# Kernel optimization log

Hardware: AMD Instinct MI355X
Metric: run time of the kernel (lower is better)

Reference implementation:

```python
import jax, jax.numpy as jnp
import numpy as np

DIM = 1024
CTX_DIM = 1024
HEADS = 16
HEAD_DIM = DIM // HEADS


def setup_inputs() -> dict:
    key = jax.random.key(0)
    ks = jax.random.split(key, 6)
    B, N, M = 2, 2048, 2048
    s = 0.02
    return {
        "x": jax.random.normal(ks[0], (B, N, DIM), dtype=jnp.float32),
        "context": jax.random.normal(ks[1], (B, M, CTX_DIM), dtype=jnp.float32),
        "W_q": jax.random.normal(ks[2], (DIM, DIM), dtype=jnp.float32) * s,
        "W_kv": jax.random.normal(ks[3], (CTX_DIM * 2, CTX_DIM), dtype=jnp.float32) * s,
        "W_proj": jax.random.normal(ks[4], (DIM, DIM), dtype=jnp.float32) * s,
        "b_proj": jax.random.normal(ks[5], (DIM,), dtype=jnp.float32) * s,
    }


def reference(x, context, W_q, W_kv, W_proj, b_proj):
    B, N, C = x.shape
    M = context.shape[1]
    scale = HEAD_DIM ** (-0.5)
    # q projection: [B,N,H,D]
    q = (x @ W_q.T).reshape(B, N, HEADS, HEAD_DIM) * scale
    # context kv projection: [B,M,2,H,D]
    kv = (context @ W_kv.T).reshape(B, M, 2, HEADS, HEAD_DIM)
    k = kv[:, :, 0]  # [B,M,H,D]
    v = kv[:, :, 0]  # NOTE: source uses qkv_context[0] for BOTH k and v (faithful)
    attn = jnp.einsum("bnhd,bmhd->bhnm", q, k)
    attn = jax.nn.softmax(attn, axis=-1)
    out = jnp.einsum("bhnm,bmhd->bnhd", attn, v).reshape(B, N, C)
    return out @ W_proj.T + b_proj
```

## Files before the change

### kernel.cpp

```cpp
#include <hip/hip_runtime.h>
#include <hip/hip_bf16.h>


typedef __bf16 bf16x8 __attribute__((ext_vector_type(8)));
typedef float f32x4 __attribute__((ext_vector_type(4)));
typedef float f32x16 __attribute__((ext_vector_type(16)));

static constexpr int kDIM = 1024;
static constexpr float kLog2e = 1.4426950408889634f;

__device__ inline unsigned short f2bf(float f) {
    union { float f; unsigned int u; } v; v.f = f;
    return (unsigned short)((v.u + 0x7FFFu + ((v.u >> 16) & 1u)) >> 16);
}

__device__ inline unsigned int pack2bf(float a, float b) {
    union { float f; unsigned int u; } ua, ub;
    ua.f = a; ub.f = b;
    return __builtin_amdgcn_perm(ub.u + 0x8000u, ua.u + 0x8000u, 0x07060302u);
}

__device__ inline void gload_lds16(const unsigned short* g, unsigned short* l) {
    __builtin_amdgcn_global_load_lds(
        (const __attribute__((address_space(1))) unsigned int*)g,
        (__attribute__((address_space(3))) unsigned int*)l, 16, 0, 0);
}

__global__ __launch_bounds__(256) void cast_all(
    const float* __restrict__ x, const float* __restrict__ ctx,
    const float* __restrict__ wq, const float* __restrict__ wkv,
    const float* __restrict__ wp,
    unsigned short* __restrict__ xb, unsigned short* __restrict__ cb,
    unsigned short* __restrict__ wqb, unsigned short* __restrict__ wkb,
    unsigned short* __restrict__ wpb)
{
    int j = blockIdx.x * 256 + threadIdx.x;
    const float* s; unsigned short* d;
    if (j < 1048576)                      { s = x;   d = xb;  }
    else if ((j -= 1048576) < 1048576)    { s = ctx; d = cb;  }
    else if ((j -= 1048576) < 262144)     { s = wq;  d = wqb; }
    else if ((j -= 262144) < 262144)      { s = wkv; d = wkb; }
    else if ((j -= 262144) < 262144)      { s = wp;  d = wpb; }
    else return;
    float4 f = ((const float4*)s)[j];
    ushort4 o;
    o.x = f2bf(f.x); o.y = f2bf(f.y); o.z = f2bf(f.z); o.w = f2bf(f.w);
    ((ushort4*)d)[j] = o;
}

__global__ __launch_bounds__(256, 4) void gemm_qk(
    const unsigned short* __restrict__ xb, const unsigned short* __restrict__ cb,
    const unsigned short* __restrict__ Wq, const unsigned short* __restrict__ Wkv,
    unsigned short* __restrict__ Qb, unsigned short* __restrict__ Kb,
    unsigned short* __restrict__ Ktb, float qscale, int Mctx)
{
    __shared__ unsigned short As[128 * 64];
    __shared__ unsigned short Bs[64 * 64];
    const int z = blockIdx.z;
    const unsigned short* A  = z ? cb : xb;
    const unsigned short* Bw = z ? Wkv : Wq;
    unsigned short* Cb = z ? Kb : Qb;
    const float scale = z ? 1.0f : qscale;

    const int tid = threadIdx.x;
    const int wave = tid >> 6, lane = tid & 63;
    const int g = lane >> 4, c = lane & 15;
    const int wm = (wave & 1) * 64, wn = (wave >> 1) * 32;
    const int bm = blockIdx.y * 128, bn = blockIdx.x * 64;

    const int srow = lane >> 3;
    const int scolsw = ((lane & 7) ^ (srow & 7)) * 8;
    const int x7 = c & 7;

    f32x4 acc[4][2];
    #pragma unroll
    for (int i = 0; i < 4; ++i)
        #pragma unroll
        for (int j = 0; j < 2; ++j)
            acc[i][j] = (f32x4){0.f, 0.f, 0.f, 0.f};

    for (int k0 = 0; k0 < kDIM; k0 += 64) {
        __syncthreads();
        #pragma unroll
        for (int t = 0; t < 4; ++t) {
            const int chunk = wave * 4 + t;
            gload_lds16(A + (size_t)(bm + chunk * 8 + srow) * kDIM + k0 + scolsw,
                        &As[chunk * 512]);
        }
        #pragma unroll
        for (int t = 0; t < 2; ++t) {
            const int chunk = wave * 2 + t;
            gload_lds16(Bw + (size_t)(bn + chunk * 8 + srow) * kDIM + k0 + scolsw,
                        &Bs[chunk * 512]);
        }
        __syncthreads();
        #pragma unroll
        for (int kc = 0; kc < 2; ++kc) {
            bf16x8 af[4], bfr[2];
            #pragma unroll
            for (int i = 0; i < 4; ++i)
                af[i] = *(const bf16x8*)&As[(wm + i * 16 + c) * 64 +
                                            ((kc * 4 + g) ^ x7) * 8];
            #pragma unroll
            for (int j = 0; j < 2; ++j)
                bfr[j] = *(const bf16x8*)&Bs[(wn + j * 16 + c) * 64 +
                                             ((kc * 4 + g) ^ x7) * 8];
            #pragma unroll
            for (int i = 0; i < 4; ++i)
                #pragma unroll
                for (int j = 0; j < 2; ++j)
                    acc[i][j] = __builtin_amdgcn_mfma_f32_16x16x32_bf16(
                        af[i], bfr[j], acc[i][j], 0, 0, 0);
        }
    }

    #pragma unroll
    for (int i = 0; i < 4; ++i) {
        #pragma unroll
        for (int j = 0; j < 2; ++j) {
            const int r0 = bm + wm + i * 16 + 4 * g;
            const int cc = bn + wn + j * 16 + c;
            float v0 = acc[i][j][0] * scale;
            float v1 = acc[i][j][1] * scale;
            float v2 = acc[i][j][2] * scale;
            float v3 = acc[i][j][3] * scale;
            Cb[(size_t)(r0 + 0) * kDIM + cc] = f2bf(v0);
            Cb[(size_t)(r0 + 1) * kDIM + cc] = f2bf(v1);
            Cb[(size_t)(r0 + 2) * kDIM + cc] = f2bf(v2);
            Cb[(size_t)(r0 + 3) * kDIM + cc] = f2bf(v3);
            if (z) {
                const int bb = r0 / Mctx, n0 = r0 % Mctx;
                const int hh = cc >> 6, d = cc & 63;
                ushort4 pk;
                pk.x = f2bf(v0); pk.y = f2bf(v1); pk.z = f2bf(v2); pk.w = f2bf(v3);
                *(ushort4*)&Ktb[((size_t)((bb * 16 + hh) * 64 + d)) * Mctx + n0] = pk;
            }
        }
    }
}

__global__ __launch_bounds__(256, 4) void gemm_proj(
    const unsigned short* __restrict__ Ab, const unsigned short* __restrict__ Wp,
    const float* __restrict__ bias, float* __restrict__ out)
{
    __shared__ unsigned short As[64 * 64];
    __shared__ unsigned short Bs[64 * 64];
    const int tid = threadIdx.x;
    const int wave = tid >> 6, lane = tid & 63;
    const int g = lane >> 4, c = lane & 15;
    const int wm = (wave & 1) * 32, wn = (wave >> 1) * 32;
    const int bm = blockIdx.y * 64, bn = blockIdx.x * 64;

    const int srow = lane >> 3;
    const int scolsw = ((lane & 7) ^ (srow & 7)) * 8;
    const int x7 = c & 7;

    f32x4 acc[2][2];
    #pragma unroll
    for (int i = 0; i < 2; ++i)
        #pragma unroll
        for (int j = 0; j < 2; ++j)
            acc[i][j] = (f32x4){0.f, 0.f, 0.f, 0.f};

    for (int k0 = 0; k0 < kDIM; k0 += 64) {
        __syncthreads();
        #pragma unroll
        for (int t = 0; t < 2; ++t) {
            const int chunk = wave * 2 + t;
            const int row = chunk * 8 + srow;
            gload_lds16(Ab + (size_t)(bm + row) * kDIM + k0 + scolsw, &As[chunk * 512]);
            gload_lds16(Wp + (size_t)(bn + row) * kDIM + k0 + scolsw, &Bs[chunk * 512]);
        }
        __syncthreads();
        #pragma unroll
        for (int kc = 0; kc < 2; ++kc) {
            bf16x8 af[2], bfr[2];
            #pragma unroll
            for (int i = 0; i < 2; ++i)
                af[i] = *(const bf16x8*)&As[(wm + i * 16 + c) * 64 +
                                            ((kc * 4 + g) ^ x7) * 8];
            #pragma unroll
            for (int j = 0; j < 2; ++j)
                bfr[j] = *(const bf16x8*)&Bs[(wn + j * 16 + c) * 64 +
                                             ((kc * 4 + g) ^ x7) * 8];
            #pragma unroll
            for (int i = 0; i < 2; ++i)
                #pragma unroll
                for (int j = 0; j < 2; ++j)
                    acc[i][j] = __builtin_amdgcn_mfma_f32_16x16x32_bf16(
                        af[i], bfr[j], acc[i][j], 0, 0, 0);
        }
    }

    #pragma unroll
    for (int i = 0; i < 2; ++i) {
        #pragma unroll
        for (int j = 0; j < 2; ++j) {
            const int r0 = bm + wm + i * 16 + 4 * g;
            const int cc = bn + wn + j * 16 + c;
            const float bv = bias[cc];
            #pragma unroll
            for (int ii = 0; ii < 4; ++ii)
                out[(size_t)(r0 + ii) * kDIM + cc] = acc[i][j][ii] + bv;
        }
    }
}

__global__ __launch_bounds__(512, 4) void attn_mfma_v5(
    const unsigned short* __restrict__ Q,
    const unsigned short* __restrict__ K,
    const unsigned short* __restrict__ Kt,
    unsigned short* __restrict__ O, int N, int M)
{
    __shared__ unsigned short smem[18432];
    unsigned short* Ks  = smem;
    unsigned short* Kts = smem + 64 * 72;
    unsigned short* Ps  = smem + 2 * 64 * 72;

    const int b = blockIdx.z, h = blockIdx.y, q0 = blockIdx.x * 128;
    const int tid = threadIdx.x;
    const int w = tid >> 6, lane = tid & 63;
    const int strip = w >> 1, kh = w & 1;
    const int ql = lane & 31, l5 = lane >> 5;

    const unsigned short* Qrow = Q + (size_t)(b * N + q0 + strip * 32 + ql) * kDIM + h * 64;
    const unsigned short* Kb = K + (size_t)b * M * kDIM + h * 64;
    const unsigned short* Ktb = Kt + (size_t)((b * 16 + h) * 64) * M;

    bf16x8 bq[4];
    #pragma unroll
    for (int kc = 0; kc < 4; ++kc)
        bq[kc] = *(const bf16x8*)(Qrow + kc * 16 + l5 * 8);

    f32x16 ot[2];
    #pragma unroll
    for (int dt = 0; dt < 2; ++dt)
        #pragma unroll
        for (int r = 0; r < 16; ++r) ot[dt][r] = 0.f;
    float lac = 0.f;

    const int srow = tid >> 3, scol = (tid & 7) * 8;
    unsigned short* prow = &Ps[(strip * 32 + ql) * 72 + kh * 32];

    for (int k0 = 0; k0 < M; k0 += 64) {
        __syncthreads();
        *(uint4*)&Ks[srow * 72 + scol] =
            *(const uint4*)(Kb + (size_t)(k0 + srow) * kDIM + scol);
        *(uint4*)&Kts[srow * 72 + scol] =
            *(const uint4*)(Ktb + (size_t)srow * M + k0 + scol);
        __syncthreads();

        f32x16 st;
        #pragma unroll
        for (int r = 0; r < 16; ++r) st[r] = 0.f;
        #pragma unroll
        for (int kc = 0; kc < 4; ++kc) {
            bf16x8 ak = *(const bf16x8*)&Ks[(kh * 32 + ql) * 72 + kc * 16 + l5 * 8];
            st = __builtin_amdgcn_mfma_f32_32x32x16_bf16(ak, bq[kc], st, 0, 0, 0);
        }

        float pr[16];
        #pragma unroll
        for (int r = 0; r < 16; ++r) {
            pr[r] = __builtin_amdgcn_exp2f(st[r]);
            lac += pr[r];
        }
        unsigned int dw[8];
        #pragma unroll
        for (int p = 0; p < 8; ++p) dw[p] = pack2bf(pr[2 * p], pr[2 * p + 1]);
        #pragma unroll
        for (int pp = 0; pp < 4; ++pp)
            *(uint2*)&prow[8 * pp + 4 * l5] = make_uint2(dw[2 * pp], dw[2 * pp + 1]);

        #pragma unroll
        for (int kc2 = 0; kc2 < 2; ++kc2) {
            bf16x8 bp = *(const bf16x8*)&prow[kc2 * 16 + l5 * 8];
            #pragma unroll
            for (int dt = 0; dt < 2; ++dt) {
                bf16x8 av = *(const bf16x8*)&Kts[(dt * 32 + ql) * 72 + kh * 32 + kc2 * 16 + l5 * 8];
                ot[dt] = __builtin_amdgcn_mfma_f32_32x32x16_bf16(av, bp, ot[dt], 0, 0, 0);
            }
        }
    }

    float lw = lac + __shfl_xor(lac, 32);
    float* Om = (float*)smem;
    float* Lm = Om + 128 * 68;
    const int qi = strip * 32 + ql;

    __syncthreads();
    if (kh == 1) {
        #pragma unroll
        for (int dt = 0; dt < 2; ++dt)
            #pragma unroll
            for (int rr = 0; rr < 4; ++rr)
                *(f32x4*)&Om[qi * 68 + dt * 32 + 8 * rr + 4 * l5] =
                    (f32x4){ot[dt][4 * rr], ot[dt][4 * rr + 1],
                            ot[dt][4 * rr + 2], ot[dt][4 * rr + 3]};
        if (l5 == 0) Lm[qi] = lw;
    }
    __syncthreads();
    if (kh == 0) {
        const float inv = 1.0f / (lw + Lm[qi]);
        unsigned short* Ob = O + (size_t)(b * N + q0 + qi) * kDIM + h * 64;
        #pragma unroll
        for (int dt = 0; dt < 2; ++dt)
            #pragma unroll
            for (int rr = 0; rr < 4; ++rr) {
                f32x4 pv = *(const f32x4*)&Om[qi * 68 + dt * 32 + 8 * rr + 4 * l5];
                ushort4 u;
                u.x = f2bf((ot[dt][4 * rr]     + pv[0]) * inv);
                u.y = f2bf((ot[dt][4 * rr + 1] + pv[1]) * inv);
                u.z = f2bf((ot[dt][4 * rr + 2] + pv[2]) * inv);
                u.w = f2bf((ot[dt][4 * rr + 3] + pv[3]) * inv);
                *(ushort4*)(Ob + dt * 32 + 8 * rr + 4 * l5) = u;
            }
    }
}

extern "C" void kernel_launch(void* const* d_in, const int* in_sizes, int n_in,
                              void* d_out, int out_size, void* d_ws, size_t ws_size,
                              hipStream_t stream)
{
    const float* x      = (const float*)d_in[0];
    const float* ctxp   = (const float*)d_in[1];
    const float* W_q    = (const float*)d_in[2];
    const float* W_kv   = (const float*)d_in[3];
    const float* W_proj = (const float*)d_in[4];
    const float* b_proj = (const float*)d_in[5];
    float* out = (float*)d_out;

    const int B = 2, N = 2048, M = 2048;
    const int BN = B * N;
    const int SQ = kDIM * kDIM;

    unsigned short* p = (unsigned short*)d_ws;
    unsigned short* xb  = p; p += (size_t)BN * kDIM;
    unsigned short* cb  = p; p += (size_t)BN * kDIM;
    unsigned short* wqb = p; p += SQ;
    unsigned short* wkb = p; p += SQ;
    unsigned short* wpb = p; p += SQ;
    unsigned short* Qb  = p; p += (size_t)BN * kDIM;
    unsigned short* Kb  = p; p += (size_t)BN * kDIM;
    unsigned short* Ktb = p; p += (size_t)BN * kDIM;
    unsigned short* Ab  = xb;

    hipLaunchKernelGGL(cast_all, dim3(11264), dim3(256), 0, stream,
                       x, ctxp, W_q, W_kv, W_proj, xb, cb, wqb, wkb, wpb);
    hipLaunchKernelGGL(gemm_qk, dim3(kDIM / 64, BN / 128, 2), dim3(256), 0, stream,
                       xb, cb, wqb, wkb, Qb, Kb, Ktb, 0.125f * kLog2e, M);
    hipLaunchKernelGGL(attn_mfma_v5, dim3(N / 128, 16, B), dim3(512), 0, stream,
                       Qb, Kb, Ktb, Ab, N, M);
    hipLaunchKernelGGL(gemm_proj, dim3(kDIM / 64, BN / 64), dim3(256), 0, stream,
                       Ab, wpb, b_proj, out);
}
```

Measured before the change: 187.1 us.

## Prefetch attention K tiles into registers, enlarge proj GEMM tile, use hardware bf16 pack

The attention kernel now loads the next K and K-transposed tiles into registers while the current tile is being computed, so global load latency can overlap the MFMA work. The output projection GEMM moves to 128x64 block tiles, which gives more MFMAs per B-tile load but launches half as many blocks. The bf16 packing of probabilities switches from a manual round-and-permute to the v_cvt_pk_bf16_f32 instruction, which also changes rounding from round-half-up to round-to-nearest-even. These edits are independent and together add register pressure.

```diff
diff --git a/kernel.cpp b/kernel.cpp
--- a/kernel.cpp
+++ b/kernel.cpp
@@ -14,10 +14,10 @@
     return (unsigned short)((v.u + 0x7FFFu + ((v.u >> 16) & 1u)) >> 16);
 }
 
-__device__ inline unsigned int pack2bf(float a, float b) {
-    union { float f; unsigned int u; } ua, ub;
-    ua.f = a; ub.f = b;
-    return __builtin_amdgcn_perm(ub.u + 0x8000u, ua.u + 0x8000u, 0x07060302u);
+__device__ inline unsigned int cvtpk2bf(float a, float b) {
+    unsigned int r;
+    asm("v_cvt_pk_bf16_f32 %0, %1, %2" : "=v"(r) : "v"(a), "v"(b));
+    return r;
 }
 
 __device__ inline void gload_lds16(const unsigned short* g, unsigned short* l) {
@@ -143,21 +143,21 @@
     const unsigned short* __restrict__ Ab, const unsigned short* __restrict__ Wp,
     const float* __restrict__ bias, float* __restrict__ out)
 {
-    __shared__ unsigned short As[64 * 64];
+    __shared__ unsigned short As[128 * 64];
     __shared__ unsigned short Bs[64 * 64];
     const int tid = threadIdx.x;
     const int wave = tid >> 6, lane = tid & 63;
     const int g = lane >> 4, c = lane & 15;
-    const int wm = (wave & 1) * 32, wn = (wave >> 1) * 32;
-    const int bm = blockIdx.y * 64, bn = blockIdx.x * 64;
+    const int wm = (wave & 1) * 64, wn = (wave >> 1) * 32;
+    const int bm = blockIdx.y * 128, bn = blockIdx.x * 64;
 
     const int srow = lane >> 3;
     const int scolsw = ((lane & 7) ^ (srow & 7)) * 8;
     const int x7 = c & 7;
 
-    f32x4 acc[2][2];
-    #pragma unroll
-    for (int i = 0; i < 2; ++i)
+    f32x4 acc[4][2];
+    #pragma unroll
+    for (int i = 0; i < 4; ++i)
         #pragma unroll
         for (int j = 0; j < 2; ++j)
             acc[i][j] = (f32x4){0.f, 0.f, 0.f, 0.f};
@@ -165,18 +165,23 @@
     for (int k0 = 0; k0 < kDIM; k0 += 64) {
         __syncthreads();
         #pragma unroll
+        for (int t = 0; t < 4; ++t) {
+            const int chunk = wave * 4 + t;
+            gload_lds16(Ab + (size_t)(bm + chunk * 8 + srow) * kDIM + k0 + scolsw,
+                        &As[chunk * 512]);
+        }
+        #pragma unroll
         for (int t = 0; t < 2; ++t) {
             const int chunk = wave * 2 + t;
-            const int row = chunk * 8 + srow;
-            gload_lds16(Ab + (size_t)(bm + row) * kDIM + k0 + scolsw, &As[chunk * 512]);
-            gload_lds16(Wp + (size_t)(bn + row) * kDIM + k0 + scolsw, &Bs[chunk * 512]);
+            gload_lds16(Wp + (size_t)(bn + chunk * 8 + srow) * kDIM + k0 + scolsw,
+                        &Bs[chunk * 512]);
         }
         __syncthreads();
         #pragma unroll
         for (int kc = 0; kc < 2; ++kc) {
-            bf16x8 af[2], bfr[2];
-            #pragma unroll
-            for (int i = 0; i < 2; ++i)
+            bf16x8 af[4], bfr[2];
+            #pragma unroll
+            for (int i = 0; i < 4; ++i)
                 af[i] = *(const bf16x8*)&As[(wm + i * 16 + c) * 64 +
                                             ((kc * 4 + g) ^ x7) * 8];
             #pragma unroll
@@ -184,7 +189,7 @@
                 bfr[j] = *(const bf16x8*)&Bs[(wn + j * 16 + c) * 64 +
                                              ((kc * 4 + g) ^ x7) * 8];
             #pragma unroll
-            for (int i = 0; i < 2; ++i)
+            for (int i = 0; i < 4; ++i)
                 #pragma unroll
                 for (int j = 0; j < 2; ++j)
                     acc[i][j] = __builtin_amdgcn_mfma_f32_16x16x32_bf16(
@@ -193,7 +198,7 @@
     }
 
     #pragma unroll
-    for (int i = 0; i < 2; ++i) {
+    for (int i = 0; i < 4; ++i) {
         #pragma unroll
         for (int j = 0; j < 2; ++j) {
             const int r0 = bm + wm + i * 16 + 4 * g;
@@ -206,7 +211,7 @@
     }
 }
 
-__global__ __launch_bounds__(512, 4) void attn_mfma_v5(
+__global__ __launch_bounds__(512, 4) void attn_mfma_v6(
     const unsigned short* __restrict__ Q,
     const unsigned short* __restrict__ K,
     const unsigned short* __restrict__ Kt,
@@ -242,13 +247,19 @@
     const int srow = tid >> 3, scol = (tid & 7) * 8;
     unsigned short* prow = &Ps[(strip * 32 + ql) * 72 + kh * 32];
 
+    uint4 rk  = *(const uint4*)(Kb  + (size_t)srow * kDIM + scol);
+    uint4 rkt = *(const uint4*)(Ktb + (size_t)srow * M + scol);
+
     for (int k0 = 0; k0 < M; k0 += 64) {
         __syncthreads();
-        *(uint4*)&Ks[srow * 72 + scol] =
-            *(const uint4*)(Kb + (size_t)(k0 + srow) * kDIM + scol);
-        *(uint4*)&Kts[srow * 72 + scol] =
-            *(const uint4*)(Ktb + (size_t)srow * M + k0 + scol);
-        __syncthreads();
+        *(uint4*)&Ks[srow * 72 + scol]  = rk;
+        *(uint4*)&Kts[srow * 72 + scol] = rkt;
+        __syncthreads();
+
+        if (k0 + 64 < M) {
+            rk  = *(const uint4*)(Kb  + (size_t)(k0 + 64 + srow) * kDIM + scol);
+            rkt = *(const uint4*)(Ktb + (size_t)srow * M + (k0 + 64) + scol);
+        }
 
         f32x16 st;
         #pragma unroll
@@ -267,7 +278,7 @@
         }
         unsigned int dw[8];
         #pragma unroll
-        for (int p = 0; p < 8; ++p) dw[p] = pack2bf(pr[2 * p], pr[2 * p + 1]);
+        for (int p = 0; p < 8; ++p) dw[p] = cvtpk2bf(pr[2 * p], pr[2 * p + 1]);
         #pragma unroll
         for (int pp = 0; pp < 4; ++pp)
             *(uint2*)&prow[8 * pp + 4 * l5] = make_uint2(dw[2 * pp], dw[2 * pp + 1]);
@@ -349,8 +360,8 @@
                        x, ctxp, W_q, W_kv, W_proj, xb, cb, wqb, wkb, wpb);
     hipLaunchKernelGGL(gemm_qk, dim3(kDIM / 64, BN / 128, 2), dim3(256), 0, stream,
                        xb, cb, wqb, wkb, Qb, Kb, Ktb, 0.125f * kLog2e, M);
-    hipLaunchKernelGGL(attn_mfma_v5, dim3(N / 128, 16, B), dim3(512), 0, stream,
+    hipLaunchKernelGGL(attn_mfma_v6, dim3(N / 128, 16, B), dim3(512), 0, stream,
                        Qb, Kb, Ktb, Ab, N, M);
-    hipLaunchKernelGGL(gemm_proj, dim3(kDIM / 64, BN / 64), dim3(256), 0, stream,
+    hipLaunchKernelGGL(gemm_proj, dim3(kDIM / 64, BN / 128), dim3(256), 0, stream,
                        Ab, wpb, b_proj, out);
 }
```

Result: no change. 186.7 us (-0.2%).

## Double-buffer GEMM LDS loads, prefetch attention K tiles, remap blocks across XCDs

Applied to the files above, without the earlier changes.

Both GEMM kernels now double-buffer their LDS tiles, issuing the next k-slice's global-to-LDS loads before computing on the current one, with one barrier per iteration instead of two. The attention kernel prefetches the next K and K-transpose tiles into registers while the current tile is being computed. All three kernels remap the linear block index so that consecutive blocks, which are likely spread across XCDs, work on neighbouring tiles, aiming for better L2 reuse. The attention kernel also swaps the manual bf16 pack for the v_cvt_pk_bf16_f32 instruction. The cost is double the LDS use in the GEMMs, which may lower occupancy, and extra registers in the attention kernel.

```diff
diff --git a/kernel.cpp b/kernel.cpp
--- a/kernel.cpp
+++ b/kernel.cpp
@@ -14,10 +14,10 @@
     return (unsigned short)((v.u + 0x7FFFu + ((v.u >> 16) & 1u)) >> 16);
 }
 
-__device__ inline unsigned int pack2bf(float a, float b) {
-    union { float f; unsigned int u; } ua, ub;
-    ua.f = a; ub.f = b;
-    return __builtin_amdgcn_perm(ub.u + 0x8000u, ua.u + 0x8000u, 0x07060302u);
+__device__ inline unsigned int cvtpk2bf(float a, float b) {
+    unsigned int r;
+    asm("v_cvt_pk_bf16_f32 %0, %1, %2" : "=v"(r) : "v"(a), "v"(b));
+    return r;
 }
 
 __device__ inline void gload_lds16(const unsigned short* g, unsigned short* l) {
@@ -54,9 +54,15 @@
     unsigned short* __restrict__ Qb, unsigned short* __restrict__ Kb,
     unsigned short* __restrict__ Ktb, float qscale, int Mctx)
 {
-    __shared__ unsigned short As[128 * 64];
-    __shared__ unsigned short Bs[64 * 64];
-    const int z = blockIdx.z;
+    __shared__ unsigned short As[2 * 128 * 64];
+    __shared__ unsigned short Bs[2 * 64 * 64];
+
+    const int lin  = blockIdx.x + 16 * blockIdx.y + 512 * blockIdx.z;
+    const int orig = (lin & 7) * 128 + (lin >> 3);
+    const int bxi  = orig & 15;
+    const int byi  = (orig >> 4) & 31;
+    const int z    = orig >> 9;
+
     const unsigned short* A  = z ? cb : xb;
     const unsigned short* Bw = z ? Wkv : Wq;
     unsigned short* Cb = z ? Kb : Qb;
@@ -66,7 +72,7 @@
     const int wave = tid >> 6, lane = tid & 63;
     const int g = lane >> 4, c = lane & 15;
     const int wm = (wave & 1) * 64, wn = (wave >> 1) * 32;
-    const int bm = blockIdx.y * 128, bn = blockIdx.x * 64;
+    const int bm = byi * 128, bn = bxi * 64;
 
     const int srow = lane >> 3;
     const int scolsw = ((lane & 7) ^ (srow & 7)) * 8;
@@ -79,31 +85,41 @@
         for (int j = 0; j < 2; ++j)
             acc[i][j] = (f32x4){0.f, 0.f, 0.f, 0.f};
 
-    for (int k0 = 0; k0 < kDIM; k0 += 64) {
-        __syncthreads();
+    auto stage = [&](int buf, int k0) {
+        unsigned short* Ad = As + buf * (128 * 64);
+        unsigned short* Bd = Bs + buf * (64 * 64);
         #pragma unroll
         for (int t = 0; t < 4; ++t) {
             const int chunk = wave * 4 + t;
             gload_lds16(A + (size_t)(bm + chunk * 8 + srow) * kDIM + k0 + scolsw,
-                        &As[chunk * 512]);
+                        Ad + chunk * 512);
         }
         #pragma unroll
         for (int t = 0; t < 2; ++t) {
             const int chunk = wave * 2 + t;
             gload_lds16(Bw + (size_t)(bn + chunk * 8 + srow) * kDIM + k0 + scolsw,
-                        &Bs[chunk * 512]);
-        }
-        __syncthreads();
+                        Bd + chunk * 512);
+        }
+    };
+
+    stage(0, 0);
+    __syncthreads();
+
+    for (int t = 0; t < 16; ++t) {
+        const int cur = t & 1;
+        if (t < 15) stage(cur ^ 1, (t + 1) * 64);
+        const unsigned short* Ac = As + cur * (128 * 64);
+        const unsigned short* Bc = Bs + cur * (64 * 64);
         #pragma unroll
         for (int kc = 0; kc < 2; ++kc) {
             bf16x8 af[4], bfr[2];
             #pragma unroll
             for (int i = 0; i < 4; ++i)
-                af[i] = *(const bf16x8*)&As[(wm + i * 16 + c) * 64 +
+                af[i] = *(const bf16x8*)&Ac[(wm + i * 16 + c) * 64 +
                                             ((kc * 4 + g) ^ x7) * 8];
             #pragma unroll
             for (int j = 0; j < 2; ++j)
-                bfr[j] = *(const bf16x8*)&Bs[(wn + j * 16 + c) * 64 +
+                bfr[j] = *(const bf16x8*)&Bc[(wn + j * 16 + c) * 64 +
                                              ((kc * 4 + g) ^ x7) * 8];
             #pragma unroll
             for (int i = 0; i < 4; ++i)
@@ -112,6 +128,7 @@
                     acc[i][j] = __builtin_amdgcn_mfma_f32_16x16x32_bf16(
                         af[i], bfr[j], acc[i][j], 0, 0, 0);
         }
+        __syncthreads();
     }
 
     #pragma unroll
@@ -143,13 +160,17 @@
     const unsigned short* __restrict__ Ab, const unsigned short* __restrict__ Wp,
     const float* __restrict__ bias, float* __restrict__ out)
 {
-    __shared__ unsigned short As[64 * 64];
-    __shared__ unsigned short Bs[64 * 64];
+    __shared__ unsigned short As[2 * 64 * 64];
+    __shared__ unsigned short Bs[2 * 64 * 64];
+
+    const int lin  = blockIdx.x + 16 * blockIdx.y;
+    const int orig = (lin & 7) * 128 + (lin >> 3);
+    const int bm = (orig >> 4) * 64, bn = (orig & 15) * 64;
+
     const int tid = threadIdx.x;
     const int wave = tid >> 6, lane = tid & 63;
     const int g = lane >> 4, c = lane & 15;
     const int wm = (wave & 1) * 32, wn = (wave >> 1) * 32;
-    const int bm = blockIdx.y * 64, bn = blockIdx.x * 64;
 
     const int srow = lane >> 3;
     const int scolsw = ((lane & 7) ^ (srow & 7)) * 8;
@@ -162,26 +183,36 @@
         for (int j = 0; j < 2; ++j)
             acc[i][j] = (f32x4){0.f, 0.f, 0.f, 0.f};
 
-    for (int k0 = 0; k0 < kDIM; k0 += 64) {
-        __syncthreads();
+    auto stage = [&](int buf, int k0) {
+        unsigned short* Ad = As + buf * (64 * 64);
+        unsigned short* Bd = Bs + buf * (64 * 64);
         #pragma unroll
         for (int t = 0; t < 2; ++t) {
             const int chunk = wave * 2 + t;
             const int row = chunk * 8 + srow;
-            gload_lds16(Ab + (size_t)(bm + row) * kDIM + k0 + scolsw, &As[chunk * 512]);
-            gload_lds16(Wp + (size_t)(bn + row) * kDIM + k0 + scolsw, &Bs[chunk * 512]);
-        }
-        __syncthreads();
+            gload_lds16(Ab + (size_t)(bm + row) * kDIM + k0 + scolsw, Ad + chunk * 512);
+            gload_lds16(Wp + (size_t)(bn + row) * kDIM + k0 + scolsw, Bd + chunk * 512);
+        }
+    };
+
+    stage(0, 0);
+    __syncthreads();
+
+    for (int t = 0; t < 16; ++t) {
+        const int cur = t & 1;
+        if (t < 15) stage(cur ^ 1, (t + 1) * 64);
+        const unsigned short* Ac = As + cur * (64 * 64);
+        const unsigned short* Bc = Bs + cur * (64 * 64);
         #pragma unroll
         for (int kc = 0; kc < 2; ++kc) {
             bf16x8 af[2], bfr[2];
             #pragma unroll
             for (int i = 0; i < 2; ++i)
-                af[i] = *(const bf16x8*)&As[(wm + i * 16 + c) * 64 +
+                af[i] = *(const bf16x8*)&Ac[(wm + i * 16 + c) * 64 +
                                             ((kc * 4 + g) ^ x7) * 8];
             #pragma unroll
             for (int j = 0; j < 2; ++j)
-                bfr[j] = *(const bf16x8*)&Bs[(wn + j * 16 + c) * 64 +
+                bfr[j] = *(const bf16x8*)&Bc[(wn + j * 16 + c) * 64 +
                                              ((kc * 4 + g) ^ x7) * 8];
             #pragma unroll
             for (int i = 0; i < 2; ++i)
@@ -190,6 +221,7 @@
                     acc[i][j] = __builtin_amdgcn_mfma_f32_16x16x32_bf16(
                         af[i], bfr[j], acc[i][j], 0, 0, 0);
         }
+        __syncthreads();
     }
 
     #pragma unroll
@@ -206,7 +238,7 @@
     }
 }
 
-__global__ __launch_bounds__(512, 4) void attn_mfma_v5(
+__global__ __launch_bounds__(512, 4) void attn_mfma_v7(
     const unsigned short* __restrict__ Q,
     const unsigned short* __restrict__ K,
     const unsigned short* __restrict__ Kt,
@@ -217,7 +249,12 @@
     unsigned short* Kts = smem + 64 * 72;
     unsigned short* Ps  = smem + 2 * 64 * 72;
 
-    const int b = blockIdx.z, h = blockIdx.y, q0 = blockIdx.x * 128;
+    const int lin  = blockIdx.x + 16 * (blockIdx.y + 16 * blockIdx.z);
+    const int orig = (lin & 7) * 64 + (lin >> 3);
+    const int q0 = (orig & 15) * 128;
+    const int h  = (orig >> 4) & 15;
+    const int b  = orig >> 8;
+
     const int tid = threadIdx.x;
     const int w = tid >> 6, lane = tid & 63;
     const int strip = w >> 1, kh = w & 1;
@@ -242,13 +279,19 @@
     const int srow = tid >> 3, scol = (tid & 7) * 8;
     unsigned short* prow = &Ps[(strip * 32 + ql) * 72 + kh * 32];
 
+    uint4 rk  = *(const uint4*)(Kb  + (size_t)srow * kDIM + scol);
+    uint4 rkt = *(const uint4*)(Ktb + (size_t)srow * M + scol);
+
     for (int k0 = 0; k0 < M; k0 += 64) {
         __syncthreads();
-        *(uint4*)&Ks[srow * 72 + scol] =
-            *(const uint4*)(Kb + (size_t)(k0 + srow) * kDIM + scol);
-        *(uint4*)&Kts[srow * 72 + scol] =
-            *(const uint4*)(Ktb + (size_t)srow * M + k0 + scol);
+        *(uint4*)&Ks[srow * 72 + scol]  = rk;
+        *(uint4*)&Kts[srow * 72 + scol] = rkt;
         __syncthreads();
+
+        if (k0 + 64 < M) {
+            rk  = *(const uint4*)(Kb  + (size_t)(k0 + 64 + srow) * kDIM + scol);
+            rkt = *(const uint4*)(Ktb + (size_t)srow * M + (k0 + 64) + scol);
+        }
 
         f32x16 st;
         #pragma unroll
@@ -267,7 +310,7 @@
         }
         unsigned int dw[8];
         #pragma unroll
-        for (int p = 0; p < 8; ++p) dw[p] = pack2bf(pr[2 * p], pr[2 * p + 1]);
+        for (int p = 0; p < 8; ++p) dw[p] = cvtpk2bf(pr[2 * p], pr[2 * p + 1]);
         #pragma unroll
         for (int pp = 0; pp < 4; ++pp)
             *(uint2*)&prow[8 * pp + 4 * l5] = make_uint2(dw[2 * pp], dw[2 * pp + 1]);
@@ -349,7 +392,7 @@
                        x, ctxp, W_q, W_kv, W_proj, xb, cb, wqb, wkb, wpb);
     hipLaunchKernelGGL(gemm_qk, dim3(kDIM / 64, BN / 128, 2), dim3(256), 0, stream,
                        xb, cb, wqb, wkb, Qb, Kb, Ktb, 0.125f * kLog2e, M);
-    hipLaunchKernelGGL(attn_mfma_v5, dim3(N / 128, 16, B), dim3(512), 0, stream,
+    hipLaunchKernelGGL(attn_mfma_v7, dim3(N / 128, 16, B), dim3(512), 0, stream,
                        Qb, Kb, Ktb, Ab, N, M);
     hipLaunchKernelGGL(gemm_proj, dim3(kDIM / 64, BN / 64), dim3(256), 0, stream,
                        Ab, wpb, b_proj, out);
```

New measurement: 194.9 us. 1.04x slower.
